# Kernel optimization log

Hardware: AMD Instinct MI355X
Metric: run time of the kernel (lower is better)

Reference implementation:

```python
import jax, jax.numpy as jnp
import numpy as np

EMBED_DIM = 256
NUM_HEADS = 8
HEAD_DIM = 32
INNER = NUM_HEADS * HEAD_DIM
NEG_SLOPE = 0.2


def setup_inputs() -> dict:
    key = jax.random.key(0)
    ks = jax.random.split(key, 8)
    B, Ns, Nt = 8, 1024, 1024
    src = jax.random.normal(ks[0], (B, Ns, EMBED_DIM), dtype=jnp.float32)
    trg = jax.random.normal(ks[1], (B, Nt, EMBED_DIM), dtype=jnp.float32)
    src_mask = jnp.ones((B, Ns), dtype=bool)
    trg_mask = jax.random.randint(ks[2], (B, Nt), 0, 2).astype(bool)
    # learned params (xavier-ish scale)
    def xavier(k, shape):
        fan_in, fan_out = shape[0], shape[-1]
        lim = (6.0 / (fan_in + fan_out)) ** 0.5
        return jax.random.uniform(k, shape, jnp.float32, -lim, lim)
    W_src = xavier(ks[3], (EMBED_DIM, INNER))
    W_trg = xavier(ks[4], (EMBED_DIM, INNER))  # is_cross_type=True -> independent
    a_src = xavier(ks[5], (NUM_HEADS, HEAD_DIM))
    a_trg = xavier(ks[6], (NUM_HEADS, HEAD_DIM))
    W_out = xavier(ks[7], (INNER, EMBED_DIM))
    return {"src": src, "trg": trg, "src_mask": src_mask, "trg_mask": trg_mask,
            "W_src": W_src, "W_trg": W_trg, "a_src": a_src, "a_trg": a_trg, "W_out": W_out}


def reference(src, trg, src_mask, trg_mask, W_src, W_trg, a_src, a_trg, W_out):
    B, Ns, _ = src.shape
    Nt = trg.shape[1]
    NH, Dh = NUM_HEADS, HEAD_DIM
    src_proj = (src @ W_src).reshape(B, Ns, NH, Dh)  # dropout p=0
    trg_proj = (trg @ W_trg).reshape(B, Nt, NH, Dh)
    score_src = jnp.einsum('bshd,hd->bsh', src_proj, a_src)
    score_trg = jnp.einsum('bthd,hd->bth', trg_proj, a_trg)
    # (B,Ns,NH,1) + (B,1,NH,Nt) -> (B,Ns,NH,Nt)
    scores = score_src[:, :, :, None] + jnp.transpose(score_trg, (0, 2, 1))[:, None, :, :]
    scores = jnp.where(scores >= 0, scores, NEG_SLOPE * scores)  # LeakyReLU
    edge_mask = src_mask[:, :, None, None] & trg_mask[:, None, None, :]
    scores = jnp.where(edge_mask, scores, -jnp.inf)
    attn = jax.nn.softmax(scores, axis=-1)
    attn = jnp.nan_to_num(attn, nan=0.0)
    aggregated = jnp.einsum('bsht,bthd->bshd', attn, trg_proj)
    output = aggregated.reshape(B, Ns, NH * Dh) @ W_out
    return output, jnp.transpose(attn, (0, 2, 1, 3))
```

## Files before the change

### kernel.cpp

```cpp
#include <hip/hip_runtime.h>
#include <hip/hip_bf16.h>
#include <math.h>

#define NB 8
#define NS 1024
#define NT 1024
#define NE 256
#define NHEADS 8
#define DH 32

typedef __attribute__((ext_vector_type(8))) short short8;
typedef __attribute__((ext_vector_type(8))) unsigned short ushort8;
typedef __attribute__((ext_vector_type(4))) float f32x4;

#define O_VT    0u
#define O_AGGB  (4u<<20)
#define O_WTT   (8u<<20)
#define O_WTO   ((8u<<20)+131072u)
#define O_CSRC  ((8u<<20)+262144u)
#define O_CTRG  (O_CSRC+8192u)
#define O_SSRC  (O_CTRG+8192u)
#define O_STRG  (O_SSRC+262144u)
#define O_FLAG  (O_STRG+262144u)

__device__ __forceinline__ unsigned short f2bf(float f) {
    __hip_bfloat16 h = __float2bfloat16(f);
    union { __hip_bfloat16 h; unsigned short u; } c; c.h = h;
    return c.u;
}
__device__ __forceinline__ float bf2f(unsigned short u) {
    union { unsigned u; float f; } x; x.u = ((unsigned)u) << 16;
    return x.f;
}

__global__ __launch_bounds__(256) void setup_kernel(
    const unsigned* __restrict__ tmask_dw, const float* __restrict__ Wsrc,
    const float* __restrict__ Wtrg, const float* __restrict__ Wout,
    const float* __restrict__ asrc, const float* __restrict__ atrg,
    float* __restrict__ c_src, float* __restrict__ c_trg,
    unsigned short* __restrict__ Wt_t, unsigned short* __restrict__ Wt_o,
    int* __restrict__ flag) {
    __shared__ __align__(16) char sm[16640];
    const int tid = threadIdx.x;
    const int bid = blockIdx.x;

    if (bid == 0) {
        __shared__ int s_ok;
        if (tid == 0) s_ok = 1;
        __syncthreads();
        for (int i = tid; i < 2048; i += 256)
            if (tmask_dw[i] > 1u) s_ok = 0;
        __syncthreads();
        if (tid == 0) *flag = s_ok;
    } else if (bid <= 2) {
        float* a_sh = (float*)sm;
        const float* W = (bid == 1) ? Wsrc : Wtrg;
        const float* a = (bid == 1) ? asrc : atrg;
        float* c = (bid == 1) ? c_src : c_trg;
        a_sh[tid] = a[tid];
        __syncthreads();
        const int e = tid;
        float ch[8];
#pragma unroll
        for (int h = 0; h < 8; ++h) ch[h] = 0.f;
        for (int i = 0; i < 64; ++i) {
            const float4 wv = *(const float4*)&W[(size_t)e * NE + i * 4];
            const int h = i >> 3, d0 = (i & 7) * 4;
            ch[h] += wv.x * a_sh[h * 32 + d0] + wv.y * a_sh[h * 32 + d0 + 1] +
                     wv.z * a_sh[h * 32 + d0 + 2] + wv.w * a_sh[h * 32 + d0 + 3];
        }
#pragma unroll
        for (int h = 0; h < 8; ++h) c[h * NE + e] = ch[h];
    } else {
        const int q = bid - 3;
        const float* W = (q >> 4) ? Wout : Wtrg;
        unsigned short* Wt = (q >> 4) ? Wt_o : Wt_t;
        const int tl = q & 15;
        const int k0 = (tl >> 2) * 64, n0 = (tl & 3) * 64;
        float* xs = (float*)sm;
#pragma unroll
        for (int it = 0; it < 4; ++it) {
            const int slot = it * 256 + tid;
            const int k = slot >> 4, c4 = slot & 15;
            const float4 v = *(const float4*)&W[(size_t)(k0 + k) * NE + n0 + c4 * 4];
            float* p = &xs[k * 65 + c4 * 4];
            p[0] = v.x; p[1] = v.y; p[2] = v.z; p[3] = v.w;
        }
        __syncthreads();
#pragma unroll
        for (int it = 0; it < 2; ++it) {
            const int slot = it * 256 + tid;
            const int n = slot >> 3, kc = slot & 7;
            ushort8 v;
#pragma unroll
            for (int e = 0; e < 8; ++e)
                v[e] = f2bf(xs[(kc * 8 + e) * 65 + n]);
            *(ushort8*)&Wt[(size_t)(n0 + n) * NE + k0 + kc * 8] = v;
        }
    }
}

__global__ __launch_bounds__(256) void mid_kernel(
    const float* __restrict__ src, const float* __restrict__ trg,
    const float* __restrict__ c_src, const float* __restrict__ c_trg,
    const unsigned short* __restrict__ Wt_t, unsigned short* __restrict__ Vt,
    float* __restrict__ ssrc, float* __restrict__ strg) {
    __shared__ __align__(16) char sm[49152];
    const int tid = threadIdx.x;
    const int bid = blockIdx.x;

    if (bid < 256) {
        unsigned short* As = (unsigned short*)sm;
        unsigned short* ldsT = (unsigned short*)(sm + 32768);
        const int lane = tid & 63, w = tid >> 6;
        const int row0 = (bid >> 1) * 64;
        const int col0 = (bid & 1) * 128;

#pragma unroll
        for (int it = 0; it < 8; ++it) {
            const int gf = it * 256 + tid;
            const int row = gf >> 5, g3 = gf & 31;
            const float4 a = *(const float4*)&trg[(size_t)(row0 + row) * NE + g3 * 8];
            const float4 b = *(const float4*)&trg[(size_t)(row0 + row) * NE + g3 * 8 + 4];
            ushort8 v;
            v[0] = f2bf(a.x); v[1] = f2bf(a.y); v[2] = f2bf(a.z); v[3] = f2bf(a.w);
            v[4] = f2bf(b.x); v[5] = f2bf(b.y); v[6] = f2bf(b.z); v[7] = f2bf(b.w);
            *(ushort8*)&As[row * NE + ((g3 ^ (row & 7)) * 8)] = v;
        }
        __syncthreads();

        const int r = lane & 15, g = lane >> 4;
        short8 af[8];
#pragma unroll
        for (int kk = 0; kk < 8; ++kk)
            af[kk] = *(const short8*)&As[(w * 16 + r) * NE + (((kk * 4 + g) ^ (r & 7)) * 8)];

        f32x4 acc[8];
#pragma unroll
        for (int nt = 0; nt < 8; ++nt) acc[nt] = (f32x4){0.f, 0.f, 0.f, 0.f};
#pragma unroll
        for (int kk = 0; kk < 8; ++kk) {
#pragma unroll
            for (int nt = 0; nt < 8; ++nt) {
                const int col = col0 + nt * 16 + r;
                const short8 bf = *(const short8*)&Wt_t[(size_t)col * NE + kk * 32 + g * 8];
                acc[nt] = __builtin_amdgcn_mfma_f32_16x16x32_bf16(af[kk], bf, acc[nt], 0, 0, 0);
            }
        }
        __syncthreads();

#pragma unroll
        for (int nt = 0; nt < 8; ++nt) {
            const int cl = nt * 16 + r;
            const int sw = (cl & 7) << 3;
#pragma unroll
            for (int j = 0; j < 4; ++j) {
                const int t = w * 16 + g * 4 + j;
                ldsT[cl * 64 + (t ^ sw)] = f2bf(acc[nt][j]);
            }
        }
        __syncthreads();

        const int b = row0 >> 10, t0 = row0 & 1023;
#pragma unroll
        for (int it = 0; it < 4; ++it) {
            const int slot = it * 256 + tid;
            const int cl = slot >> 3, ch = slot & 7;
            const int colg = col0 + cl;
            const int h = colg >> 5, d = colg & 31;
            *(ushort8*)&Vt[(((size_t)(b * 8 + h)) * 32 + d) * 1024 + t0 + ch * 8] =
                *(const ushort8*)&ldsT[cl * 64 + ch * 8];
        }
    } else {
        float* xs = (float*)sm;
        float* cs = (float*)(sm + 32768);
        const int rowg0 = (bid - 256) * 32;
        const bool is_src = rowg0 < NB * NS;
        const float* X = is_src ? (src + (size_t)rowg0 * NE)
                                : (trg + (size_t)(rowg0 - NB * NS) * NE);
        const float* C = is_src ? c_src : c_trg;
        float* S = is_src ? (ssrc + (size_t)rowg0 * NHEADS)
                          : (strg + (size_t)(rowg0 - NB * NS) * NHEADS);

#pragma unroll
        for (int it = 0; it < 8; ++it) {
            const int slot = it * 256 + tid;
            const int row = slot >> 6, c4 = slot & 63;
            *(float4*)&xs[row * NE + c4 * 4] =
                *(const float4*)&X[(size_t)row * NE + c4 * 4];
            cs[slot] = C[slot];
        }
        __syncthreads();

        const int r = tid >> 3, h = tid & 7;
        float s = 0.f;
        for (int e = 0; e < NE; e += 4) {
            const float4 x = *(const float4*)&xs[r * NE + e];
            const float4 c = *(const float4*)&cs[h * NE + e];
            s += x.x * c.x + x.y * c.y + x.z * c.z + x.w * c.w;
        }
        S[(size_t)r * NHEADS + h] = s;
    }
}

__global__ __launch_bounds__(256) void fused_softmax_agg_kernel(
    const float* __restrict__ ssrc, const float* __restrict__ strg,
    const void* __restrict__ smask, const void* __restrict__ tmask,
    const int* __restrict__ flag_p, const unsigned short* __restrict__ Vt,
    float* __restrict__ attn, unsigned short* __restrict__ agg_bf) {
    const int blk = blockIdx.x;
    const int stile = blk & 15;
    const int h = (blk >> 4) & 7;
    const int b = blk >> 7;
    const int tid = threadIdx.x;
    const int lane = tid & 63;
    const int wave = tid >> 6;
    const int flag = *flag_p;

    __shared__ __align__(16) float s_sm[NT];
    __shared__ float s_inv[64];

    for (int t = tid; t < NT; t += 256) {
        const bool mv = flag ? (((const int*)tmask)[b * NT + t] != 0)
                             : (((const unsigned char*)tmask)[b * NT + t] != 0);
        s_sm[t] = mv ? strg[((size_t)b * NT + t) * NHEADS + h] : -1e30f;
    }
    __syncthreads();

    const int r = lane & 15;
    const int g = lane >> 4;
    const int srow = stile * 64 + wave * 16 + r;
    const float ss = ssrc[((size_t)b * NS + srow) * NHEADS + h];
    const bool rowv = flag ? (((const int*)smask)[b * NS + srow] != 0)
                           : (((const unsigned char*)smask)[b * NS + srow] != 0);
    const int sw = (r & 7) << 3;
    const unsigned short* vr0 = Vt + (size_t)(b * NHEADS + h) * 32768 + r * 1024;
    const unsigned short* vr1 = vr0 + 16 * 1024;

    float sum = 0.f;
#pragma unroll 4
    for (int c = 0; c < 32; ++c) {
        const int tb = c * 32 + g * 8;
        const float4 v0 = *(const float4*)&s_sm[tb];
        const float4 v1 = *(const float4*)&s_sm[tb + 4];
        const float vv[8] = {v0.x, v0.y, v0.z, v0.w, v1.x, v1.y, v1.z, v1.w};
#pragma unroll
        for (int e = 0; e < 8; ++e) {
            float v = ss + vv[e];
            v = (v >= 0.f) ? v : 0.2f * v;
            sum += __expf(v);
        }
    }
    sum += __shfl_xor(sum, 16);
    sum += __shfl_xor(sum, 32);
    const float inv = (rowv && sum > 0.f) ? 1.f / sum : 0.f;
    if (g == 0) s_inv[wave * 16 + r] = inv;

    f32x4 acc0 = {0.f, 0.f, 0.f, 0.f};
    f32x4 acc1 = {0.f, 0.f, 0.f, 0.f};
    float* arow = attn + ((size_t)((b * NHEADS + h) * NS) + srow) * NT;

#pragma unroll 4
    for (int c = 0; c < 32; ++c) {
        const int tb = c * 32 + g * 8;
        const short8 b0 = *(const short8*)&vr0[tb ^ sw];
        const short8 b1 = *(const short8*)&vr1[tb ^ sw];
        const float4 v0 = *(const float4*)&s_sm[tb];
        const float4 v1 = *(const float4*)&s_sm[tb + 4];
        const float vv[8] = {v0.x, v0.y, v0.z, v0.w, v1.x, v1.y, v1.z, v1.w};
        float p[8];
        short8 pa;
#pragma unroll
        for (int e = 0; e < 8; ++e) {
            float v = ss + vv[e];
            v = (v >= 0.f) ? v : 0.2f * v;
            p[e] = __expf(v);
            pa[e] = (short)f2bf(p[e]);
        }
        const float4 o0 = {p[0] * inv, p[1] * inv, p[2] * inv, p[3] * inv};
        const float4 o1 = {p[4] * inv, p[5] * inv, p[6] * inv, p[7] * inv};
        *(float4*)(arow + tb) = o0;
        *(float4*)(arow + tb + 4) = o1;
        acc0 = __builtin_amdgcn_mfma_f32_16x16x32_bf16(pa, b0, acc0, 0, 0, 0);
        acc1 = __builtin_amdgcn_mfma_f32_16x16x32_bf16(pa, b1, acc1, 0, 0, 0);
    }

    __syncthreads();
    const int orow = stile * 64 + wave * 16 + g * 4;
    unsigned short* ab = agg_bf + ((size_t)b * NS + orow) * NE + h * DH + r;
#pragma unroll
    for (int j = 0; j < 4; ++j) {
        const float iv = s_inv[wave * 16 + g * 4 + j];
        ab[(size_t)j * NE] = f2bf(acc0[j] * iv);
        ab[(size_t)j * NE + 16] = f2bf(acc1[j] * iv);
    }
}

__global__ __launch_bounds__(256) void gemm_out_kernel(
    const unsigned short* __restrict__ Xb, const unsigned short* __restrict__ Wt,
    float* __restrict__ Yf) {
    __shared__ __align__(16) unsigned short As[64 * NE];
    const int tid = threadIdx.x;
    const int lane = tid & 63;
    const int w = tid >> 6;
    const int row0 = blockIdx.x * 64;
    const int col0 = blockIdx.y * 128;

#pragma unroll
    for (int it = 0; it < 8; ++it) {
        const int gf = it * 256 + tid;
        const int row = gf >> 5, g3 = gf & 31;
        const ushort8 v = *(const ushort8*)&Xb[(size_t)(row0 + row) * NE + g3 * 8];
        *(ushort8*)&As[row * NE + ((g3 ^ (row & 7)) * 8)] = v;
    }
    __syncthreads();

    const int r = lane & 15, g = lane >> 4;
    short8 af[8];
#pragma unroll
    for (int kk = 0; kk < 8; ++kk)
        af[kk] = *(const short8*)&As[(w * 16 + r) * NE + (((kk * 4 + g) ^ (r & 7)) * 8)];

    f32x4 acc[8];
#pragma unroll
    for (int nt = 0; nt < 8; ++nt) acc[nt] = (f32x4){0.f, 0.f, 0.f, 0.f};
#pragma unroll
    for (int kk = 0; kk < 8; ++kk) {
#pragma unroll
        for (int nt = 0; nt < 8; ++nt) {
            const int col = col0 + nt * 16 + r;
            const short8 bf = *(const short8*)&Wt[(size_t)col * NE + kk * 32 + g * 8];
            acc[nt] = __builtin_amdgcn_mfma_f32_16x16x32_bf16(af[kk], bf, acc[nt], 0, 0, 0);
        }
    }

#pragma unroll
    for (int nt = 0; nt < 8; ++nt) {
        const int col = col0 + nt * 16 + r;
#pragma unroll
        for (int j = 0; j < 4; ++j) {
            const int row = row0 + w * 16 + g * 4 + j;
            Yf[(size_t)row * NE + col] = acc[nt][j];
        }
    }
}

extern "C" void kernel_launch(void* const* d_in, const int* in_sizes, int n_in,
                              void* d_out, int out_size, void* d_ws, size_t ws_size,
                              hipStream_t stream) {
    const float* src   = (const float*)d_in[0];
    const float* trg   = (const float*)d_in[1];
    const void*  smask = d_in[2];
    const void*  tmask = d_in[3];
    const float* Wsrc  = (const float*)d_in[4];
    const float* Wtrg  = (const float*)d_in[5];
    const float* asrc  = (const float*)d_in[6];
    const float* atrg  = (const float*)d_in[7];
    const float* Wout  = (const float*)d_in[8];

    float* out  = (float*)d_out;
    float* attn = out + (size_t)NB * NS * NE;

    char* wsb = (char*)d_ws;
    unsigned short* Vt     = (unsigned short*)(wsb + O_VT);
    unsigned short* agg_bf = (unsigned short*)(wsb + O_AGGB);
    unsigned short* Wt_t   = (unsigned short*)(wsb + O_WTT);
    unsigned short* Wt_o   = (unsigned short*)(wsb + O_WTO);
    float* c_src = (float*)(wsb + O_CSRC);
    float* c_trg = (float*)(wsb + O_CTRG);
    float* ssrc  = (float*)(wsb + O_SSRC);
    float* strg  = (float*)(wsb + O_STRG);
    int*   flag  = (int*)(wsb + O_FLAG);

    setup_kernel<<<35, 256, 0, stream>>>(
        (const unsigned*)tmask, Wsrc, Wtrg, Wout, asrc, atrg,
        c_src, c_trg, Wt_t, Wt_o, flag);

    mid_kernel<<<768, 256, 0, stream>>>(
        src, trg, c_src, c_trg, Wt_t, Vt, ssrc, strg);

    fused_softmax_agg_kernel<<<NB * NHEADS * (NS / 64), 256, 0, stream>>>(
        ssrc, strg, smask, tmask, flag, Vt, attn, agg_bf);

    gemm_out_kernel<<<dim3(128, 2), 256, 0, stream>>>(agg_bf, Wt_o, out);
}
```

Baseline: 104.4 us.

## Fuse softmax sum into MFMA pass and rewrite attn stores row-coalesced

The separate pass that only computed the softmax denominator is removed. The row sum is now accumulated inside the MFMA aggregation loop and the normalization is applied afterward. The attention probabilities are then written in a second pass in which each wave stores whole rows with fully contiguous float4 accesses, replacing the earlier scattered per-lane stores. Each exponential is still computed twice, but global write coalescing for the large attention output should improve, and one loop's worth of LDS reads is removed.

```diff
diff --git a/kernel.cpp b/kernel.cpp
--- a/kernel.cpp
+++ b/kernel.cpp
@@ -31,6 +31,9 @@
 __device__ __forceinline__ float bf2f(unsigned short u) {
     union { unsigned u; float f; } x; x.u = ((unsigned)u) << 16;
     return x.f;
+}
+__device__ __forceinline__ float leaky(float v) {
+    return (v >= 0.f) ? v : 0.2f * v;
 }
 
 __global__ __launch_bounds__(256) void setup_kernel(
@@ -219,6 +222,7 @@
 
     __shared__ __align__(16) float s_sm[NT];
     __shared__ float s_inv[64];
+    __shared__ float s_ss[64];
 
     for (int t = tid; t < NT; t += 256) {
         const bool mv = flag ? (((const int*)tmask)[b * NT + t] != 0)
@@ -237,29 +241,9 @@
     const unsigned short* vr0 = Vt + (size_t)(b * NHEADS + h) * 32768 + r * 1024;
     const unsigned short* vr1 = vr0 + 16 * 1024;
 
-    float sum = 0.f;
-#pragma unroll 4
-    for (int c = 0; c < 32; ++c) {
-        const int tb = c * 32 + g * 8;
-        const float4 v0 = *(const float4*)&s_sm[tb];
-        const float4 v1 = *(const float4*)&s_sm[tb + 4];
-        const float vv[8] = {v0.x, v0.y, v0.z, v0.w, v1.x, v1.y, v1.z, v1.w};
-#pragma unroll
-        for (int e = 0; e < 8; ++e) {
-            float v = ss + vv[e];
-            v = (v >= 0.f) ? v : 0.2f * v;
-            sum += __expf(v);
-        }
-    }
-    sum += __shfl_xor(sum, 16);
-    sum += __shfl_xor(sum, 32);
-    const float inv = (rowv && sum > 0.f) ? 1.f / sum : 0.f;
-    if (g == 0) s_inv[wave * 16 + r] = inv;
-
     f32x4 acc0 = {0.f, 0.f, 0.f, 0.f};
     f32x4 acc1 = {0.f, 0.f, 0.f, 0.f};
-    float* arow = attn + ((size_t)((b * NHEADS + h) * NS) + srow) * NT;
-
+    float sum = 0.f;
 #pragma unroll 4
     for (int c = 0; c < 32; ++c) {
         const int tb = c * 32 + g * 8;
@@ -268,31 +252,55 @@
         const float4 v0 = *(const float4*)&s_sm[tb];
         const float4 v1 = *(const float4*)&s_sm[tb + 4];
         const float vv[8] = {v0.x, v0.y, v0.z, v0.w, v1.x, v1.y, v1.z, v1.w};
-        float p[8];
         short8 pa;
 #pragma unroll
         for (int e = 0; e < 8; ++e) {
-            float v = ss + vv[e];
-            v = (v >= 0.f) ? v : 0.2f * v;
-            p[e] = __expf(v);
-            pa[e] = (short)f2bf(p[e]);
-        }
-        const float4 o0 = {p[0] * inv, p[1] * inv, p[2] * inv, p[3] * inv};
-        const float4 o1 = {p[4] * inv, p[5] * inv, p[6] * inv, p[7] * inv};
-        *(float4*)(arow + tb) = o0;
-        *(float4*)(arow + tb + 4) = o1;
+            const float p = __expf(leaky(ss + vv[e]));
+            sum += p;
+            pa[e] = (short)f2bf(p);
+        }
         acc0 = __builtin_amdgcn_mfma_f32_16x16x32_bf16(pa, b0, acc0, 0, 0, 0);
         acc1 = __builtin_amdgcn_mfma_f32_16x16x32_bf16(pa, b1, acc1, 0, 0, 0);
     }
 
+    sum += __shfl_xor(sum, 16);
+    sum += __shfl_xor(sum, 32);
+    const float inv = (rowv && sum > 0.f) ? 1.f / sum : 0.f;
+    if (g == 0) {
+        s_inv[wave * 16 + r] = inv;
+        s_ss[wave * 16 + r] = ss;
+    }
     __syncthreads();
-    const int orow = stile * 64 + wave * 16 + g * 4;
-    unsigned short* ab = agg_bf + ((size_t)b * NS + orow) * NE + h * DH + r;
-#pragma unroll
-    for (int j = 0; j < 4; ++j) {
-        const float iv = s_inv[wave * 16 + g * 4 + j];
-        ab[(size_t)j * NE] = f2bf(acc0[j] * iv);
-        ab[(size_t)j * NE + 16] = f2bf(acc1[j] * iv);
+
+    {
+        const int orow = stile * 64 + wave * 16 + g * 4;
+        unsigned short* ab = agg_bf + ((size_t)b * NS + orow) * NE + h * DH + r;
+#pragma unroll
+        for (int j = 0; j < 4; ++j) {
+            const float iv = s_inv[wave * 16 + g * 4 + j];
+            ab[(size_t)j * NE] = f2bf(acc0[j] * iv);
+            ab[(size_t)j * NE + 16] = f2bf(acc1[j] * iv);
+        }
+    }
+
+    float* wbase = attn + ((size_t)((b * NHEADS + h) * NS) + stile * 64 + wave * 16) * NT;
+    const float* ssv = &s_ss[wave * 16];
+    const float* invv = &s_inv[wave * 16];
+    for (int rr = 0; rr < 16; ++rr) {
+        const float ssr = ssv[rr];
+        const float ivr = invv[rr];
+        float* arow = wbase + (size_t)rr * NT;
+#pragma unroll
+        for (int q = 0; q < 4; ++q) {
+            const int t0 = q * 256 + lane * 4;
+            const float4 sm4 = *(const float4*)&s_sm[t0];
+            float4 o;
+            o.x = __expf(leaky(ssr + sm4.x)) * ivr;
+            o.y = __expf(leaky(ssr + sm4.y)) * ivr;
+            o.z = __expf(leaky(ssr + sm4.z)) * ivr;
+            o.w = __expf(leaky(ssr + sm4.w)) * ivr;
+            *(float4*)&arow[t0] = o;
+        }
     }
 }
 
```

New measurement: 98.49 us. 1.06x faster.
